# Kernel optimization log

Measured on AMD Instinct MI355X. Metric: run time of the kernel, lower is better.

## Reference

```python
import jax, jax.numpy as jnp
import numpy as np


def _pointnet(x, w1, b1, w2, b2, w3, b3):
    # x: [B, 3, P]; shared per-point MLP 3->64->128->128, max-pool over points -> [B,128]
    h = jax.nn.relu(jnp.einsum('oc,bcp->bop', w1, x) + b1[None, :, None])
    h = jax.nn.relu(jnp.einsum('oc,bcp->bop', w2, h) + b2[None, :, None])
    h = jax.nn.relu(jnp.einsum('oc,bcp->bop', w3, h) + b3[None, :, None])
    return h.max(axis=2)


def _lstm_layer(x, wih, whh, b):
    # x: [B, T, D]; standard LSTM (pytorch gate order i,f,g,o), returns [B, T, 128]
    B = x.shape[0]
    h0 = jnp.zeros((B, 128), x.dtype)
    def step(carry, xt):
        h, c = carry
        g = xt @ wih.T + h @ whh.T + b
        i, f, gg, o = jnp.split(g, 4, axis=-1)
        c = jax.nn.sigmoid(f) * c + jax.nn.sigmoid(i) * jnp.tanh(gg)
        h = jax.nn.sigmoid(o) * jnp.tanh(c)
        return (h, c), h
    _, hs = jax.lax.scan(step, (h0, h0), jnp.swapaxes(x, 0, 1))
    return jnp.swapaxes(hs, 0, 1)


def _edgeconv(x, aff, tw, tb, pw, pb, N):
    # DGL EdgeConv, max aggregation. Edges: det i -> track (N+j) where aff[i,j]==1, plus
    # self loops on every node. Message on edge u->v: theta(x_u - x_v) + phi(x_v).
    phi = x @ pw.T + pb                                   # [N+M, 256]
    diff = x[:N][:, None, :] - x[N:][None, :, :]          # [N, M, 256] (x_src - x_dst)
    msg = jnp.einsum('nmc,oc->nmo', diff, tw) + tb        # theta applied to diffs
    msg = jnp.where(aff[:, :, None] > 0, msg, jnp.finfo(x.dtype).min)
    h_trk = phi[N:] + jnp.maximum(tb, msg.max(axis=0))    # self-loop message is theta(0)=tb
    h_det = phi[:N] + tb                                  # dets only receive their self loop
    return jnp.concatenate([h_det, h_trk], axis=0)


def _forward(det_pc_in_box, det_boxes3d, track_pc_in_box, track_boxes3d, init_aff_matrix,
             pn_w1, pn_b1, pn_w2, pn_b2, pn_w3, pn_b3,
             mlp_w1, mlp_b1, mlp_w2, mlp_b2,
             l0_wih, l0_whh, l0_b, l1_wih, l1_whh, l1_b,
             ec_tw, ec_tb, ec_pw, ec_pb,
             er_w1, er_b1, er_w2, er_b2):
    N = det_pc_in_box.shape[0]
    det_app = _pointnet(jnp.swapaxes(det_pc_in_box, 1, 2), pn_w1, pn_b1, pn_w2, pn_b2, pn_w3, pn_b3)
    trk_app = _pointnet(jnp.swapaxes(track_pc_in_box, 1, 2), pn_w1, pn_b1, pn_w2, pn_b2, pn_w3, pn_b3)
    det_mot = jax.nn.relu(det_boxes3d @ mlp_w1.T + mlp_b1) @ mlp_w2.T + mlp_b2
    trk_mot = _lstm_layer(_lstm_layer(track_boxes3d, l0_wih, l0_whh, l0_b), l1_wih, l1_whh, l1_b)[:, -1, :]
    h = jnp.concatenate([jnp.concatenate([det_app, det_mot], axis=1),
                         jnp.concatenate([trk_app, trk_mot], axis=1)], axis=0)  # [N+M, 256]
    for k in range(4):
        h = jax.nn.relu(_edgeconv(h, init_aff_matrix, ec_tw[k], ec_tb[k], ec_pw[k], ec_pb[k], N))
    # pairwise affinity: (track - det) differences through small MLP + sigmoid (BCE head)
    edges = h[N:][None, :, :] - h[:N][:, None, :]                                # [N, M, 256]
    e = jax.nn.relu(jnp.einsum('nmc,oc->nmo', edges, er_w1) + er_b1)             # [N, M, 64]
    regr = jax.nn.sigmoid(jnp.einsum('nmo,ko->nmk', e, er_w2) + er_b2)[..., 0]   # [N, M]
    valid = init_aff_matrix * regr
    valid = jnp.where(valid == 0, jnp.asarray(99.0, valid.dtype), valid)
    return valid


def setup_inputs() -> dict:
    key = jax.random.key(0)
    ks = jax.random.split(key, 20)
    N, M, P, T = 512, 512, 256, 10
    f = jnp.float32
    def rn(k, shp):
        return jax.random.normal(k, shp, dtype=f) * 0.05
    return {
        'det_pc_in_box': jax.random.normal(ks[0], (N, P, 3), dtype=f),
        'det_boxes3d': jax.random.normal(ks[1], (N, 9), dtype=f),
        'track_pc_in_box': jax.random.normal(ks[2], (M, P, 3), dtype=f),
        'track_boxes3d': jax.random.normal(ks[3], (M, T, 9), dtype=f),
        'init_aff_matrix': jnp.ones((N, M), dtype=f),
        'gt_affinity_matrix': jnp.zeros((N, M), dtype=jnp.int32),
        'pn_w1': rn(ks[4], (64, 3)), 'pn_b1': jnp.zeros((64,), f),
        'pn_w2': rn(ks[5], (128, 64)), 'pn_b2': jnp.zeros((128,), f),
        'pn_w3': rn(ks[6], (128, 128)), 'pn_b3': jnp.zeros((128,), f),
        'mlp_w1': rn(ks[7], (64, 9)), 'mlp_b1': jnp.zeros((64,), f),
        'mlp_w2': rn(ks[8], (128, 64)), 'mlp_b2': jnp.zeros((128,), f),
        'l0_wih': rn(ks[9], (512, 9)), 'l0_whh': rn(ks[10], (512, 128)), 'l0_b': jnp.zeros((512,), f),
        'l1_wih': rn(ks[11], (512, 128)), 'l1_whh': rn(ks[12], (512, 128)), 'l1_b': jnp.zeros((512,), f),
        'ec_tw': rn(ks[13], (4, 256, 256)), 'ec_tb': jnp.zeros((4, 256), f),
        'ec_pw': rn(ks[14], (4, 256, 256)), 'ec_pb': jnp.zeros((4, 256), f),
        'er_w1': rn(ks[15], (64, 256)), 'er_b1': jnp.zeros((64,), f),
        'er_w2': rn(ks[16], (1, 64)), 'er_b2': jnp.zeros((1,), f),
    }


def reference(det_pc_in_box, det_boxes3d, track_pc_in_box, track_boxes3d, init_aff_matrix,
              gt_affinity_matrix,
              pn_w1, pn_b1, pn_w2, pn_b2, pn_w3, pn_b3,
              mlp_w1, mlp_b1, mlp_w2, mlp_b2,
              l0_wih, l0_whh, l0_b, l1_wih, l1_whh, l1_b,
              ec_tw, ec_tb, ec_pw, ec_pb,
              er_w1, er_b1, er_w2, er_b2):
    # gt_affinity_matrix is only used by the training loss; inference path ignores it.
    return _forward(det_pc_in_box, det_boxes3d, track_pc_in_box, track_boxes3d, init_aff_matrix,
                    pn_w1, pn_b1, pn_w2, pn_b2, pn_w3, pn_b3,
                    mlp_w1, mlp_b1, mlp_w2, mlp_b2,
                    l0_wih, l0_whh, l0_b, l1_wih, l1_whh, l1_b,
                    ec_tw, ec_tb, ec_pw, ec_pb,
                    er_w1, er_b1, er_w2, er_b2)
```

## Files before the change

kernel.cpp:

```cpp
#include <hip/hip_runtime.h>
#include <math.h>

#define N_DET 512
#define N_TRK 512
#define NPTS  256

typedef __attribute__((ext_vector_type(8))) short short8;
typedef __attribute__((ext_vector_type(4))) float f32x4;
typedef unsigned short ushort_t;

__device__ __forceinline__ float sigm(float x) { return 1.f / (1.f + expf(-x)); }

__device__ __forceinline__ unsigned short f2bf(float f) {
    unsigned u = __float_as_uint(f);
    u += 0x7FFF + ((u >> 16) & 1);
    return (unsigned short)(u >> 16);
}
__device__ __forceinline__ float bf2f(unsigned short h) {
    return __uint_as_float(((unsigned)h) << 16);
}

__global__ __launch_bounds__(64) void pn_wprep_kernel(
    const float* __restrict__ w2, const float* __restrict__ w3,
    unsigned short* __restrict__ wfrag)
{
    const int f = blockIdx.x;
    const int lane = threadIdx.x;
    const int lm = lane & 15, lg = lane >> 4;
    const float* src;
    if (f < 16) {
        const int s = f >> 3, n = f & 7;
        src = w2 + (size_t)(n*16 + lm)*64 + s*32 + lg*8;
    } else {
        const int f2 = f - 16, s = f2 >> 3, n = f2 & 7;
        src = w3 + (size_t)(n*16 + lm)*128 + s*32 + lg*8;
    }
    short8 v;
#pragma unroll
    for (int j = 0; j < 8; ++j) v[j] = (short)f2bf(src[j]);
    *reinterpret_cast<short8*>(wfrag + ((size_t)f*64 + lane)*8) = v;
}

__global__ __launch_bounds__(64) void ec_wprep_kernel(
    const float* __restrict__ tw, const float* __restrict__ pw,
    unsigned short* __restrict__ whi, unsigned short* __restrict__ wlo)
{
    const int id = blockIdx.x;
    const int layer = id >> 8;
    const int ntile = (id >> 3) & 31, kf = id & 7;
    const int lane = threadIdx.x;
    const int lm = lane & 15, lg = lane >> 4;
    const int col = ntile*16 + lm, k = kf*32 + lg*8;
    const float* src = (col < 256)
        ? tw + ((size_t)layer*256 + col)*256 + k
        : pw + ((size_t)layer*256 + (col - 256))*256 + k;
    short8 hi, lo;
#pragma unroll
    for (int j = 0; j < 8; ++j) {
        const float f = src[j];
        const unsigned short h = f2bf(f);
        hi[j] = (short)h;
        lo[j] = (short)f2bf(f - bf2f(h));
    }
    const size_t off = ((size_t)id*64 + lane)*8;
    *reinterpret_cast<short8*>(whi + off) = hi;
    *reinterpret_cast<short8*>(wlo + off) = lo;
}

__global__ __launch_bounds__(64) void lstm_wprep_kernel(
    const float* __restrict__ whh0, const float* __restrict__ wih1,
    const float* __restrict__ whh1, unsigned short* __restrict__ wf)
{
    const int id = blockIdx.x;
    const int mat = id >> 7, rest = id & 127;
    const int nt = rest >> 2, kf = rest & 3;
    const int lane = threadIdx.x;
    const int lm = lane & 15, lg = lane >> 4;
    const float* src = (mat == 0) ? whh0 : ((mat == 1) ? wih1 : whh1);
    const float* p = src + (size_t)(nt*16 + lm)*128 + kf*32 + lg*8;
    short8 v;
#pragma unroll
    for (int j = 0; j < 8; ++j) v[j] = (short)f2bf(p[j]);
    *reinterpret_cast<short8*>(wf + ((size_t)id*64 + lane)*8) = v;
}

__global__ __launch_bounds__(512) void lstm_xg0_kernel(
    const float* __restrict__ xseq, const float* __restrict__ wih0,
    float* __restrict__ xg0)
{
    __shared__ float xs[8][12];
    const int tid = threadIdx.x;
    const int m0 = blockIdx.x * 8;
    if (tid < 72) xs[tid / 9][tid % 9] = xseq[(size_t)m0*9 + tid];
    float wx[9];
#pragma unroll
    for (int c = 0; c < 9; ++c) wx[c] = wih0[tid*9 + c];
    __syncthreads();
#pragma unroll
    for (int i = 0; i < 8; ++i) {
        float s = 0.f;
#pragma unroll
        for (int c = 0; c < 9; ++c) s = fmaf(wx[c], xs[i][c], s);
        xg0[(size_t)(m0 + i)*512 + tid] = s;
    }
}

__global__ __launch_bounds__(256) void lstm_xg1_kernel(
    const unsigned short* __restrict__ h0hi, const unsigned short* __restrict__ h0lo,
    const unsigned short* __restrict__ wfrag, float* __restrict__ xg1)
{
    const int tid = threadIdx.x, lane = tid & 63, w = tid >> 6;
    const int lm = lane & 15, lg = lane >> 4;
    const int m0 = blockIdx.x*64 + w*16;
    const int bn = blockIdx.y;
    const int arow = m0 + lm;
    short8 ahi[4], alo[4];
#pragma unroll
    for (int kf = 0; kf < 4; ++kf) {
        ahi[kf] = *reinterpret_cast<const short8*>(h0hi + (size_t)arow*128 + kf*32 + lg*8);
        alo[kf] = *reinterpret_cast<const short8*>(h0lo + (size_t)arow*128 + kf*32 + lg*8);
    }
#pragma unroll
    for (int nt = 0; nt < 4; ++nt) {
        f32x4 acc = {0.f, 0.f, 0.f, 0.f};
#pragma unroll
        for (int kf = 0; kf < 4; ++kf) {
            const short8 bf = *reinterpret_cast<const short8*>(
                wfrag + ((size_t)((bn*4 + nt)*4 + kf)*64 + lane)*8);
            acc = __builtin_amdgcn_mfma_f32_16x16x32_bf16(ahi[kf], bf, acc, 0, 0, 0);
            acc = __builtin_amdgcn_mfma_f32_16x16x32_bf16(alo[kf], bf, acc, 0, 0, 0);
        }
#pragma unroll
        for (int r = 0; r < 4; ++r)
            xg1[(size_t)(m0 + lg*4 + r)*512 + bn*64 + nt*16 + lm] = acc[r];
    }
}

template<int LAYER>
__global__ __launch_bounds__(512, 2) void lstm_mfma_kernel(
    const unsigned short* __restrict__ wfrag,
    const float* __restrict__ xg, const float* __restrict__ bias,
    unsigned short* __restrict__ h0hi, unsigned short* __restrict__ h0lo,
    float* __restrict__ hout)
{
    __shared__ unsigned short hfhi[4*64*8];
    __shared__ unsigned short hflo[4*64*8];
    __shared__ float gs[512*20];

    const int tid = threadIdx.x;
    const int lane = tid & 63, w = tid >> 6;
    const int lm = lane & 15, lg = lane >> 4;
    const int b0 = blockIdx.x * 16;

    short8 wf[4][4];
#pragma unroll
    for (int nt = 0; nt < 4; ++nt)
#pragma unroll
        for (int kf = 0; kf < 4; ++kf)
            wf[nt][kf] = *reinterpret_cast<const short8*>(
                wfrag + ((size_t)((w*4 + nt)*4 + kf)*64 + lane)*8);

    for (int i = tid; i < 2048; i += 512) { hfhi[i] = 0; hflo[i] = 0; }

    const int mj = tid & 127;
    const int mb0 = (tid >> 7) * 4;
    const float bi = bias[mj], bf_ = bias[128 + mj];
    const float bg = bias[256 + mj], bo = bias[384 + mj];
    const int hkf = mj >> 5, hlg = (mj >> 3) & 3, hjj = mj & 7;
    float c[4] = {0.f, 0.f, 0.f, 0.f};

    __syncthreads();

    for (int t = 0; t < 10; ++t) {
        float xgv[4][4];
#pragma unroll
        for (int s = 0; s < 4; ++s) {
            const size_t btg = ((size_t)(b0 + mb0 + s)*10 + t)*512;
            xgv[s][0] = xg[btg + mj];
            xgv[s][1] = xg[btg + 128 + mj];
            xgv[s][2] = xg[btg + 256 + mj];
            xgv[s][3] = xg[btg + 384 + mj];
        }
        short8 ahi[4], alo[4];
#pragma unroll
        for (int kf = 0; kf < 4; ++kf) {
            ahi[kf] = *reinterpret_cast<const short8*>(&hfhi[(kf*64 + lane)*8]);
            alo[kf] = *reinterpret_cast<const short8*>(&hflo[(kf*64 + lane)*8]);
        }
#pragma unroll
        for (int nt = 0; nt < 4; ++nt) {
            f32x4 acc = {0.f, 0.f, 0.f, 0.f};
#pragma unroll
            for (int kf = 0; kf < 4; ++kf) {
                acc = __builtin_amdgcn_mfma_f32_16x16x32_bf16(ahi[kf], wf[nt][kf], acc, 0, 0, 0);
                acc = __builtin_amdgcn_mfma_f32_16x16x32_bf16(alo[kf], wf[nt][kf], acc, 0, 0, 0);
            }
            const int g = w*64 + nt*16 + lm;
            float4 tmp; tmp.x = acc[0]; tmp.y = acc[1]; tmp.z = acc[2]; tmp.w = acc[3];
            *(float4*)&gs[g*20 + lg*4] = tmp;
        }
        __syncthreads();
#pragma unroll
        for (int s = 0; s < 4; ++s) {
            const int b = mb0 + s;
            const float gi = gs[mj*20 + b]         + xgv[s][0] + bi;
            const float gf = gs[(128 + mj)*20 + b] + xgv[s][1] + bf_;
            const float gg = gs[(256 + mj)*20 + b] + xgv[s][2] + bg;
            const float go = gs[(384 + mj)*20 + b] + xgv[s][3] + bo;
            c[s] = sigm(gf)*c[s] + sigm(gi)*tanhf(gg);
            const float hn = sigm(go)*tanhf(c[s]);
            const unsigned short hh = f2bf(hn);
            const unsigned short hl = f2bf(hn - bf2f(hh));
            hfhi[(hkf*64 + hlg*16 + b)*8 + hjj] = hh;
            hflo[(hkf*64 + hlg*16 + b)*8 + hjj] = hl;
            if constexpr (LAYER == 0) {
                h0hi[((size_t)(b0 + b)*10 + t)*128 + mj] = hh;
                h0lo[((size_t)(b0 + b)*10 + t)*128 + mj] = hl;
            } else {
                if (t == 9)
                    hout[(size_t)(N_DET + b0 + b)*256 + 128 + mj] = hn;
            }
        }
        __syncthreads();
    }
}

__global__ __launch_bounds__(256) void h2bf_kernel(
    const float* __restrict__ h,
    unsigned short* __restrict__ hi, unsigned short* __restrict__ lo)
{
    const int id = blockIdx.x * 256 + threadIdx.x;
    const float4 v = *(const float4*)(h + (size_t)id*4);
    ushort_t h4[4], l4[4];
    const float vv[4] = {v.x, v.y, v.z, v.w};
#pragma unroll
    for (int j = 0; j < 4; ++j) {
        h4[j] = f2bf(vv[j]);
        l4[j] = f2bf(vv[j] - bf2f(h4[j]));
    }
    *(ulong1*)(hi + (size_t)id*4) = *(ulong1*)h4;
    *(ulong1*)(lo + (size_t)id*4) = *(ulong1*)l4;
}

__global__ __launch_bounds__(256, 1) void pointnet_mfma_kernel(
    const float* __restrict__ det_pc, const float* __restrict__ trk_pc,
    const float* __restrict__ w1, const float* __restrict__ b1,
    const unsigned short* __restrict__ wfrag,
    const float* __restrict__ b2, const float* __restrict__ b3,
    float* __restrict__ hout)
{
    __shared__ unsigned short h1s[256*72];
    __shared__ unsigned short h2s[256*136];
    __shared__ float wmaxs[4][128];

    const int tid = threadIdx.x;
    const int box = blockIdx.x;
    const int lane = tid & 63, w = tid >> 6;
    const int lm = lane & 15, lg = lane >> 4;

    const float* pc = (box < N_DET) ? det_pc + ((size_t)box*NPTS + tid)*3
                                    : trk_pc + ((size_t)(box - N_DET)*NPTS + tid)*3;
    const float x = pc[0], y = pc[1], z = pc[2];
#pragma unroll
    for (int j = 0; j < 8; ++j) {
        short8 v;
#pragma unroll
        for (int o = 0; o < 8; ++o) {
            const int ch = j*8 + o;
            float s = fmaf(w1[ch*3+0], x, fmaf(w1[ch*3+1], y,
                        fmaf(w1[ch*3+2], z, b1[ch])));
            v[o] = (short)f2bf(fmaxf(s, 0.f));
        }
        *reinterpret_cast<short8*>(&h1s[tid*72 + j*8]) = v;
    }
    __syncthreads();

    short8 w2f[16];
#pragma unroll
    for (int f = 0; f < 16; ++f)
        w2f[f] = *reinterpret_cast<const short8*>(wfrag + ((size_t)f*64 + lane)*8);
    float b2v[8];
#pragma unroll
    for (int n = 0; n < 8; ++n) b2v[n] = b2[n*16 + lm];

#pragma unroll
    for (int t = 0; t < 4; ++t) {
        const int arow = w*64 + t*16 + lm;
        const short8 a0 = *reinterpret_cast<const short8*>(&h1s[arow*72 + lg*8]);
        const short8 a1 = *reinterpret_cast<const short8*>(&h1s[arow*72 + 32 + lg*8]);
        const int wrow = w*64 + t*16 + lg*4;
#pragma unroll
        for (int n = 0; n < 8; ++n) {
            f32x4 acc = {0.f, 0.f, 0.f, 0.f};
            acc = __builtin_amdgcn_mfma_f32_16x16x32_bf16(a0, w2f[n],     acc, 0, 0, 0);
            acc = __builtin_amdgcn_mfma_f32_16x16x32_bf16(a1, w2f[8 + n], acc, 0, 0, 0);
#pragma unroll
            for (int r = 0; r < 4; ++r) {
                const float v = fmaxf(acc[r] + b2v[n], 0.f);
                h2s[(wrow + r)*136 + n*16 + lm] = f2bf(v);
            }
        }
    }
    __syncthreads();

    short8 w3f[32];
#pragma unroll
    for (int f = 0; f < 32; ++f)
        w3f[f] = *reinterpret_cast<const short8*>(wfrag + ((size_t)(16 + f)*64 + lane)*8);

    float pm[8];
#pragma unroll
    for (int n = 0; n < 8; ++n) pm[n] = -3.0e38f;

#pragma unroll
    for (int t = 0; t < 4; ++t) {
        const int arow = w*64 + t*16 + lm;
        const short8 a0 = *reinterpret_cast<const short8*>(&h2s[arow*136 +  0 + lg*8]);
        const short8 a1 = *reinterpret_cast<const short8*>(&h2s[arow*136 + 32 + lg*8]);
        const short8 a2 = *reinterpret_cast<const short8*>(&h2s[arow*136 + 64 + lg*8]);
        const short8 a3 = *reinterpret_cast<const short8*>(&h2s[arow*136 + 96 + lg*8]);
#pragma unroll
        for (int n = 0; n < 8; ++n) {
            f32x4 acc = {0.f, 0.f, 0.f, 0.f};
            acc = __builtin_amdgcn_mfma_f32_16x16x32_bf16(a0, w3f[n],      acc, 0, 0, 0);
            acc = __builtin_amdgcn_mfma_f32_16x16x32_bf16(a1, w3f[8 + n],  acc, 0, 0, 0);
            acc = __builtin_amdgcn_mfma_f32_16x16x32_bf16(a2, w3f[16 + n], acc, 0, 0, 0);
            acc = __builtin_amdgcn_mfma_f32_16x16x32_bf16(a3, w3f[24 + n], acc, 0, 0, 0);
#pragma unroll
            for (int r = 0; r < 4; ++r) pm[n] = fmaxf(pm[n], acc[r]);
        }
    }
#pragma unroll
    for (int n = 0; n < 8; ++n) {
        float v = pm[n];
        v = fmaxf(v, __shfl_xor(v, 16, 64));
        v = fmaxf(v, __shfl_xor(v, 32, 64));
        pm[n] = v;
    }
    if (lg == 0) {
#pragma unroll
        for (int n = 0; n < 8; ++n) wmaxs[w][n*16 + lm] = pm[n];
    }
    __syncthreads();
    if (tid < 128) {
        const float m = fmaxf(fmaxf(wmaxs[0][tid], wmaxs[1][tid]),
                              fmaxf(wmaxs[2][tid], wmaxs[3][tid]));
        hout[(size_t)box*256 + tid] = fmaxf(m + b3[tid], 0.f);
    }
}

__global__ __launch_bounds__(128) void detmlp_kernel(
    const float* __restrict__ boxes,
    const float* __restrict__ w1, const float* __restrict__ b1,
    const float* __restrict__ w2, const float* __restrict__ b2,
    float* __restrict__ hout)
{
    __shared__ float xb[9];
    __shared__ float h1[64];
    const int b = blockIdx.x, t = threadIdx.x;
    if (t < 9) xb[t] = boxes[b*9 + t];
    __syncthreads();
    if (t < 64) {
        float s = b1[t];
#pragma unroll
        for (int c = 0; c < 9; ++c) s = fmaf(w1[t*9+c], xb[c], s);
        h1[t] = fmaxf(s, 0.f);
    }
    __syncthreads();
    float s = b2[t];
    const float* wr = w2 + t*64;
#pragma unroll
    for (int c = 0; c < 64; ++c) s = fmaf(wr[c], h1[c], s);
    hout[(size_t)b * 256 + 128 + t] = s;
}

__global__ __launch_bounds__(256) void ec_gemm_mfma_kernel(
    const unsigned short* __restrict__ hhi, const unsigned short* __restrict__ hlo,
    const unsigned short* __restrict__ whi, const unsigned short* __restrict__ wlo,
    const float* __restrict__ tb, const float* __restrict__ pb,
    float* __restrict__ Abuf, float* __restrict__ Bbuf,
    float* __restrict__ phiT, float* __restrict__ hnext,
    unsigned short* __restrict__ nhi, unsigned short* __restrict__ nlo)
{
    const int bm = blockIdx.x, bn = blockIdx.y;
    const int tid = threadIdx.x, lane = tid & 63, w = tid >> 6;
    const int lm = lane & 15, lg = lane >> 4;
    const int mrow0 = bm*32 + (w & 1)*16;
    const int nt0   = bn*4 + (w >> 1)*2;
    const int arow  = mrow0 + lm;

    f32x4 acc[2] = {{0.f,0.f,0.f,0.f},{0.f,0.f,0.f,0.f}};

#pragma unroll
    for (int kf = 0; kf < 8; ++kf) {
        const short8 ahi = *reinterpret_cast<const short8*>(
            hhi + (size_t)arow*256 + kf*32 + lg*8);
        const short8 alo = *reinterpret_cast<const short8*>(
            hlo + (size_t)arow*256 + kf*32 + lg*8);
#pragma unroll
        for (int n2 = 0; n2 < 2; ++n2) {
            const size_t foff = ((size_t)((nt0 + n2)*8 + kf)*64 + lane)*8;
            const short8 bhi = *reinterpret_cast<const short8*>(whi + foff);
            const short8 blo = *reinterpret_cast<const short8*>(wlo + foff);
            acc[n2] = __builtin_amdgcn_mfma_f32_16x16x32_bf16(ahi, bhi, acc[n2], 0, 0, 0);
            acc[n2] = __builtin_amdgcn_mfma_f32_16x16x32_bf16(alo, bhi, acc[n2], 0, 0, 0);
            acc[n2] = __builtin_amdgcn_mfma_f32_16x16x32_bf16(ahi, blo, acc[n2], 0, 0, 0);
        }
    }

#pragma unroll
    for (int n2 = 0; n2 < 2; ++n2) {
        const int col = (nt0 + n2)*16 + lm;
#pragma unroll
        for (int r = 0; r < 4; ++r) {
            const int row = mrow0 + lg*4 + r;
            float v = acc[n2][r];
            if (col < 256) {
                if (row < N_DET) Abuf[(size_t)row*256 + col] = v;
                else             Bbuf[(size_t)(row - N_DET)*256 + col] = v;
            } else {
                const int o = col - 256;
                v += pb[o];
                if (row < N_DET) {
                    const float hv = fmaxf(v + tb[o], 0.f);
                    hnext[(size_t)row*256 + o] = hv;
                    const unsigned short hb = f2bf(hv);
                    nhi[(size_t)row*256 + o] = hb;
                    nlo[(size_t)row*256 + o] = f2bf(hv - bf2f(hb));
                } else {
                    phiT[(size_t)(row - N_DET)*256 + o] = v;
                }
            }
        }
    }
}

#define CM_MT 16
#define CM_OT 32
#define CM_NC 64

__global__ __launch_bounds__(256) void ec_colmax_kernel(
    const float* __restrict__ aff,
    const float* __restrict__ Abuf, const float* __restrict__ Bbuf,
    const float* __restrict__ phiT, const float* __restrict__ tb,
    float* __restrict__ hnext,
    unsigned short* __restrict__ nhi, unsigned short* __restrict__ nlo)
{
    __shared__ float As[CM_NC][CM_OT + 4];
    __shared__ float Fs[CM_NC][CM_MT + 4];
    const int t = threadIdx.x;
    const int mtile = blockIdx.x;
    const int otile = blockIdx.y;
    const int mi = t >> 4, oi = t & 15;

    float mx0 = -3.0e38f, mx1 = -3.0e38f;

    for (int n0 = 0; n0 < 512; n0 += CM_NC) {
        if (n0) __syncthreads();
        {
            const int r = t >> 3, c4 = (t & 7) * 4;
#pragma unroll
            for (int rr = 0; rr < 2; ++rr) {
                const float4 v = *(const float4*)(
                    Abuf + (size_t)(n0 + rr*32 + r)*256 + otile*CM_OT + c4);
                *(float4*)&As[rr*32 + r][c4] = v;
            }
        }
        {
            const int n = t >> 2, m4 = (t & 3) * 4;
            const float4 a = *(const float4*)(
                aff + (size_t)(n0 + n)*512 + mtile*CM_MT + m4);
            float4 f;
            f.x = (a.x > 0.f) ? 0.f : -3.0e38f;
            f.y = (a.y > 0.f) ? 0.f : -3.0e38f;
            f.z = (a.z > 0.f) ? 0.f : -3.0e38f;
            f.w = (a.w > 0.f) ? 0.f : -3.0e38f;
            *(float4*)&Fs[n][m4] = f;
        }
        __syncthreads();
#pragma unroll 4
        for (int n = 0; n < CM_NC; ++n) {
            const float f = Fs[n][mi];
            const float2 a = *(const float2*)&As[n][oi*2];
            mx0 = fmaxf(mx0, a.x + f);
            mx1 = fmaxf(mx1, a.y + f);
        }
    }

    const int m = mtile*CM_MT + mi;
    const int o = otile*CM_OT + oi*2;
    const float2 tb2 = *(const float2*)(tb + o);
    const float2 bb  = *(const float2*)(Bbuf + (size_t)m*256 + o);
    const float2 ph  = *(const float2*)(phiT + (size_t)m*256 + o);
    const float v0 = fmaxf(tb2.x, mx0 - bb.x + tb2.x);
    const float v1 = fmaxf(tb2.y, mx1 - bb.y + tb2.y);
    float2 outv;
    outv.x = fmaxf(ph.x + v0, 0.f);
    outv.y = fmaxf(ph.y + v1, 0.f);
    const size_t base = (size_t)(N_DET + m)*256 + o;
    *(float2*)(hnext + base) = outv;
    const unsigned short h0 = f2bf(outv.x), h1 = f2bf(outv.y);
    nhi[base]     = h0;
    nhi[base + 1] = h1;
    nlo[base]     = f2bf(outv.x - bf2f(h0));
    nlo[base + 1] = f2bf(outv.y - bf2f(h1));
}

__global__ __launch_bounds__(256) void headp_kernel(
    const float* __restrict__ h, const float* __restrict__ w1, float* __restrict__ P)
{
    const int tid = threadIdx.x;
    const int o = tid & 63, rl = tid >> 6;
    const int row = blockIdx.x * 4 + rl;
    const float* hr = h + (size_t)row * 256;
    const float* wr = w1 + (size_t)o * 256;
    float s0 = 0.f, s1 = 0.f, s2 = 0.f, s3 = 0.f;
#pragma unroll
    for (int c = 0; c < 256; c += 4) {
        const float4 hv = *(const float4*)(hr + c);
        const float4 wv = *(const float4*)(wr + c);
        s0 = fmaf(hv.x, wv.x, s0);
        s1 = fmaf(hv.y, wv.y, s1);
        s2 = fmaf(hv.z, wv.z, s2);
        s3 = fmaf(hv.w, wv.w, s3);
    }
    P[(size_t)row * 64 + o] = (s0 + s1) + (s2 + s3);
}

__global__ __launch_bounds__(256) void pairwise_kernel(
    const float* __restrict__ P, const float* __restrict__ aff,
    const float* __restrict__ eb1, const float* __restrict__ ew2, const float* __restrict__ eb2,
    float* __restrict__ out)
{
    __shared__ float pd[64], sb1[64], sw2[64];
    const int n = blockIdx.y;
    const int t = threadIdx.x;
    if (t < 64)       pd[t]        = P[(size_t)n * 64 + t];
    else if (t < 128) sb1[t - 64]  = eb1[t - 64];
    else if (t < 192) sw2[t - 128] = ew2[t - 128];
    __syncthreads();
    const int m = blockIdx.x * 256 + t;
    const float* pt = P + (size_t)(N_DET + m) * 64;
    float s = eb2[0];
#pragma unroll
    for (int c = 0; c < 64; c += 4) {
        const float4 pv = *(const float4*)(pt + c);
        float e;
        e = fmaxf(pv.x - pd[c+0] + sb1[c+0], 0.f); s = fmaf(e, sw2[c+0], s);
        e = fmaxf(pv.y - pd[c+1] + sb1[c+1], 0.f); s = fmaf(e, sw2[c+1], s);
        e = fmaxf(pv.z - pd[c+2] + sb1[c+2], 0.f); s = fmaf(e, sw2[c+2], s);
        e = fmaxf(pv.w - pd[c+3] + sb1[c+3], 0.f); s = fmaf(e, sw2[c+3], s);
    }
    const float r = 1.f / (1.f + expf(-s));
    const float v = aff[(size_t)n * 512 + m] * r;
    out[(size_t)n * 512 + m] = (v == 0.f) ? 99.f : v;
}

extern "C" void kernel_launch(void* const* d_in, const int* in_sizes, int n_in,
                              void* d_out, int out_size, void* d_ws, size_t ws_size,
                              hipStream_t stream)
{
    (void)in_sizes; (void)n_in; (void)out_size; (void)ws_size;

    const float* det_pc  = (const float*)d_in[0];
    const float* det_box = (const float*)d_in[1];
    const float* trk_pc  = (const float*)d_in[2];
    const float* trk_box = (const float*)d_in[3];
    const float* aff     = (const float*)d_in[4];
    const float* pn_w1  = (const float*)d_in[6];
    const float* pn_b1  = (const float*)d_in[7];
    const float* pn_w2  = (const float*)d_in[8];
    const float* pn_b2  = (const float*)d_in[9];
    const float* pn_w3  = (const float*)d_in[10];
    const float* pn_b3  = (const float*)d_in[11];
    const float* mlp_w1 = (const float*)d_in[12];
    const float* mlp_b1 = (const float*)d_in[13];
    const float* mlp_w2 = (const float*)d_in[14];
    const float* mlp_b2 = (const float*)d_in[15];
    const float* l0_wih = (const float*)d_in[16];
    const float* l0_whh = (const float*)d_in[17];
    const float* l0_b   = (const float*)d_in[18];
    const float* l1_wih = (const float*)d_in[19];
    const float* l1_whh = (const float*)d_in[20];
    const float* l1_b   = (const float*)d_in[21];
    const float* ec_tw  = (const float*)d_in[22];
    const float* ec_tb  = (const float*)d_in[23];
    const float* ec_pw  = (const float*)d_in[24];
    const float* ec_pb  = (const float*)d_in[25];
    const float* er_w1  = (const float*)d_in[26];
    const float* er_b1  = (const float*)d_in[27];
    const float* er_w2  = (const float*)d_in[28];
    const float* er_b2  = (const float*)d_in[29];

    float* ws    = (float*)d_ws;
    float* hA    = ws;
    float* hB    = hA + 1024*256;
    float* Abuf  = hB + 1024*256;
    float* Bbuf  = Abuf + 512*256;
    float* phiT  = Bbuf + 512*256;
    float* P     = phiT + 512*256;
    float* xg0   = P + 1024*64;
    float* xg1   = xg0 + 5120*512;
    unsigned short* wfrag  = (unsigned short*)(xg1 + 5120*512);
    unsigned short* ecwhi  = wfrag + 48*64*8;
    unsigned short* ecwlo  = ecwhi + 1024*64*8;
    unsigned short* lstmwf = ecwlo + 1024*64*8;
    unsigned short* h0hi   = lstmwf + 3*128*64*8;
    unsigned short* h0lo   = h0hi + 5120*128;
    unsigned short* hbfA_hi = h0lo + 5120*128;
    unsigned short* hbfA_lo = hbfA_hi + 1024*256;
    unsigned short* hbfB_hi = hbfA_lo + 1024*256;
    unsigned short* hbfB_lo = hbfB_hi + 1024*256;

    pn_wprep_kernel<<<48, 64, 0, stream>>>(pn_w2, pn_w3, wfrag);
    ec_wprep_kernel<<<1024, 64, 0, stream>>>(ec_tw, ec_pw, ecwhi, ecwlo);
    lstm_wprep_kernel<<<384, 64, 0, stream>>>(l0_whh, l1_wih, l1_whh, lstmwf);
    pointnet_mfma_kernel<<<1024, 256, 0, stream>>>(det_pc, trk_pc, pn_w1, pn_b1,
                                                   wfrag, pn_b2, pn_b3, hA);
    detmlp_kernel<<<512, 128, 0, stream>>>(det_box, mlp_w1, mlp_b1, mlp_w2, mlp_b2, hA);

    lstm_xg0_kernel<<<640, 512, 0, stream>>>(trk_box, l0_wih, xg0);
    lstm_mfma_kernel<0><<<32, 512, 0, stream>>>(lstmwf, xg0, l0_b, h0hi, h0lo, nullptr);
    lstm_xg1_kernel<<<dim3(80, 8), 256, 0, stream>>>(h0hi, h0lo, lstmwf + 128*64*8, xg1);
    lstm_mfma_kernel<1><<<32, 512, 0, stream>>>(lstmwf + 2*128*64*8, xg1, l1_b,
                                                nullptr, nullptr, hA);

    h2bf_kernel<<<256, 256, 0, stream>>>(hA, hbfA_hi, hbfA_lo);

    float* hcur = hA;  float* hnext = hB;
    unsigned short* chi = hbfA_hi; unsigned short* clo = hbfA_lo;
    unsigned short* nhi = hbfB_hi; unsigned short* nlo = hbfB_lo;
    for (int k = 0; k < 4; ++k) {
        const float* tb = ec_tb + (size_t)k * 256;
        const float* pb = ec_pb + (size_t)k * 256;
        ec_gemm_mfma_kernel<<<dim3(32, 8), 256, 0, stream>>>(
            chi, clo, ecwhi + (size_t)k*256*64*8, ecwlo + (size_t)k*256*64*8,
            tb, pb, Abuf, Bbuf, phiT, hnext, nhi, nlo);
        ec_colmax_kernel<<<dim3(32, 8), 256, 0, stream>>>(aff, Abuf, Bbuf, phiT, tb,
                                                          hnext, nhi, nlo);
        float* tf = hcur; hcur = hnext; hnext = tf;
        unsigned short* th = chi; chi = nhi; nhi = th;
        unsigned short* tl = clo; clo = nlo; nlo = tl;
    }

    headp_kernel<<<256, 256, 0, stream>>>(hcur, er_w1, P);
    pairwise_kernel<<<dim3(2, 512), 256, 0, stream>>>(P, aff, er_b1, er_w2, er_b2,
                                                      (float*)d_out);
}
```

Measured before the change: 349.3 us.

## Fuse PointNet layers per 16-point tile to shrink LDS and raise occupancy

Shrinks the PointNet kernel's shared memory from full 256-point buffers to small per-wave 16-row tiles. Layer 1 now lives in packed registers, and layer 2 and layer 3 are interleaved within each tile loop. W3 fragments are reloaded from global/cache per tile instead of held in 32 registers, and the launch bound no longer forces one block per CU. The aim is more concurrent blocks for latency hiding, at the cost of extra barriers per tile and repeated weight loads.

```diff
diff --git a/kernel.cpp b/kernel.cpp
--- a/kernel.cpp
+++ b/kernel.cpp
@@ -242,15 +242,15 @@
     *(ulong1*)(lo + (size_t)id*4) = *(ulong1*)l4;
 }
 
-__global__ __launch_bounds__(256, 1) void pointnet_mfma_kernel(
+__global__ __launch_bounds__(256) void pointnet_mfma_kernel(
     const float* __restrict__ det_pc, const float* __restrict__ trk_pc,
     const float* __restrict__ w1, const float* __restrict__ b1,
     const unsigned short* __restrict__ wfrag,
     const float* __restrict__ b2, const float* __restrict__ b3,
     float* __restrict__ hout)
 {
-    __shared__ unsigned short h1s[256*72];
-    __shared__ unsigned short h2s[256*136];
+    __shared__ unsigned short h1t[4][16][72];
+    __shared__ unsigned short h2t[4][16][136];
     __shared__ float wmaxs[4][128];
 
     const int tid = threadIdx.x;
@@ -261,19 +261,14 @@
     const float* pc = (box < N_DET) ? det_pc + ((size_t)box*NPTS + tid)*3
                                     : trk_pc + ((size_t)(box - N_DET)*NPTS + tid)*3;
     const float x = pc[0], y = pc[1], z = pc[2];
-#pragma unroll
-    for (int j = 0; j < 8; ++j) {
-        short8 v;
-#pragma unroll
-        for (int o = 0; o < 8; ++o) {
-            const int ch = j*8 + o;
-            float s = fmaf(w1[ch*3+0], x, fmaf(w1[ch*3+1], y,
-                        fmaf(w1[ch*3+2], z, b1[ch])));
-            v[o] = (short)f2bf(fmaxf(s, 0.f));
-        }
-        *reinterpret_cast<short8*>(&h1s[tid*72 + j*8]) = v;
-    }
-    __syncthreads();
+    unsigned h1p[32];
+#pragma unroll
+    for (int j = 0; j < 32; ++j) {
+        const int c0 = 2*j, c1 = 2*j + 1;
+        float s0 = fmaf(w1[c0*3+0], x, fmaf(w1[c0*3+1], y, fmaf(w1[c0*3+2], z, b1[c0])));
+        float s1 = fmaf(w1[c1*3+0], x, fmaf(w1[c1*3+1], y, fmaf(w1[c1*3+2], z, b1[c1])));
+        h1p[j] = (unsigned)f2bf(fmaxf(s0, 0.f)) | ((unsigned)f2bf(fmaxf(s1, 0.f)) << 16);
+    }
 
     short8 w2f[16];
 #pragma unroll
@@ -283,12 +278,24 @@
 #pragma unroll
     for (int n = 0; n < 8; ++n) b2v[n] = b2[n*16 + lm];
 
-#pragma unroll
+    float pm[8];
+#pragma unroll
+    for (int n = 0; n < 8; ++n) pm[n] = -3.0e38f;
+
     for (int t = 0; t < 4; ++t) {
-        const int arow = w*64 + t*16 + lm;
-        const short8 a0 = *reinterpret_cast<const short8*>(&h1s[arow*72 + lg*8]);
-        const short8 a1 = *reinterpret_cast<const short8*>(&h1s[arow*72 + 32 + lg*8]);
-        const int wrow = w*64 + t*16 + lg*4;
+        __syncthreads();
+        if (lg == t) {
+#pragma unroll
+            for (int q = 0; q < 8; ++q) {
+                uint4 v;
+                v.x = h1p[q*4+0]; v.y = h1p[q*4+1];
+                v.z = h1p[q*4+2]; v.w = h1p[q*4+3];
+                *(uint4*)&h1t[w][lm][q*8] = v;
+            }
+        }
+        __syncthreads();
+        const short8 a0 = *reinterpret_cast<const short8*>(&h1t[w][lm][lg*8]);
+        const short8 a1 = *reinterpret_cast<const short8*>(&h1t[w][lm][32 + lg*8]);
 #pragma unroll
         for (int n = 0; n < 8; ++n) {
             f32x4 acc = {0.f, 0.f, 0.f, 0.f};
@@ -297,39 +304,30 @@
 #pragma unroll
             for (int r = 0; r < 4; ++r) {
                 const float v = fmaxf(acc[r] + b2v[n], 0.f);
-                h2s[(wrow + r)*136 + n*16 + lm] = f2bf(v);
+                h2t[w][lg*4 + r][n*16 + lm] = f2bf(v);
             }
         }
-    }
-    __syncthreads();
-
-    short8 w3f[32];
-#pragma unroll
-    for (int f = 0; f < 32; ++f)
-        w3f[f] = *reinterpret_cast<const short8*>(wfrag + ((size_t)(16 + f)*64 + lane)*8);
-
-    float pm[8];
-#pragma unroll
-    for (int n = 0; n < 8; ++n) pm[n] = -3.0e38f;
-
-#pragma unroll
-    for (int t = 0; t < 4; ++t) {
-        const int arow = w*64 + t*16 + lm;
-        const short8 a0 = *reinterpret_cast<const short8*>(&h2s[arow*136 +  0 + lg*8]);
-        const short8 a1 = *reinterpret_cast<const short8*>(&h2s[arow*136 + 32 + lg*8]);
-        const short8 a2 = *reinterpret_cast<const short8*>(&h2s[arow*136 + 64 + lg*8]);
-        const short8 a3 = *reinterpret_cast<const short8*>(&h2s[arow*136 + 96 + lg*8]);
+        __syncthreads();
+        const short8 c0 = *reinterpret_cast<const short8*>(&h2t[w][lm][  0 + lg*8]);
+        const short8 c1 = *reinterpret_cast<const short8*>(&h2t[w][lm][ 32 + lg*8]);
+        const short8 c2 = *reinterpret_cast<const short8*>(&h2t[w][lm][ 64 + lg*8]);
+        const short8 c3 = *reinterpret_cast<const short8*>(&h2t[w][lm][ 96 + lg*8]);
 #pragma unroll
         for (int n = 0; n < 8; ++n) {
             f32x4 acc = {0.f, 0.f, 0.f, 0.f};
-            acc = __builtin_amdgcn_mfma_f32_16x16x32_bf16(a0, w3f[n],      acc, 0, 0, 0);
-            acc = __builtin_amdgcn_mfma_f32_16x16x32_bf16(a1, w3f[8 + n],  acc, 0, 0, 0);
-            acc = __builtin_amdgcn_mfma_f32_16x16x32_bf16(a2, w3f[16 + n], acc, 0, 0, 0);
-            acc = __builtin_amdgcn_mfma_f32_16x16x32_bf16(a3, w3f[24 + n], acc, 0, 0, 0);
+            const short8 b0f = *reinterpret_cast<const short8*>(wfrag + ((size_t)(16 +      n)*64 + lane)*8);
+            const short8 b1f = *reinterpret_cast<const short8*>(wfrag + ((size_t)(16 +  8 + n)*64 + lane)*8);
+            const short8 b2f = *reinterpret_cast<const short8*>(wfrag + ((size_t)(16 + 16 + n)*64 + lane)*8);
+            const short8 b3f = *reinterpret_cast<const short8*>(wfrag + ((size_t)(16 + 24 + n)*64 + lane)*8);
+            acc = __builtin_amdgcn_mfma_f32_16x16x32_bf16(c0, b0f, acc, 0, 0, 0);
+            acc = __builtin_amdgcn_mfma_f32_16x16x32_bf16(c1, b1f, acc, 0, 0, 0);
+            acc = __builtin_amdgcn_mfma_f32_16x16x32_bf16(c2, b2f, acc, 0, 0, 0);
+            acc = __builtin_amdgcn_mfma_f32_16x16x32_bf16(c3, b3f, acc, 0, 0, 0);
 #pragma unroll
             for (int r = 0; r < 4; ++r) pm[n] = fmaxf(pm[n], acc[r]);
         }
     }
+
 #pragma unroll
     for (int n = 0; n < 8; ++n) {
         float v = pm[n];
```

Result: no change. 349.3 us (+0.0%).
